# Optimization experiments

Hardware: AMD Instinct MI355X
Metric: run time of the kernel (lower is better)

## Reference

```python
import jax, jax.numpy as jnp
import numpy as np

N_NODES = 100000
N_EDGES = 1600000
IN_F = 128
HID_F = 128
OUT_F = 128
HEAD_HID = 128
HEAD_OUT = 64


def setup_inputs() -> dict:
    key = jax.random.key(0)
    ks = jax.random.split(key, 16)
    glorot = lambda k, i, o: jax.random.normal(k, (i, o), jnp.float32) * (2.0 / (i + o)) ** 0.5
    return {
        "x": jax.random.normal(ks[0], (N_NODES, IN_F), jnp.float32),
        "src": jax.random.randint(ks[1], (N_EDGES,), 0, N_NODES),
        "dst": jax.random.randint(ks[2], (N_EDGES,), 0, N_NODES),
        "eps1": jnp.zeros((), jnp.float32),
        "eps2": jnp.zeros((), jnp.float32),
        # mlp_fun1: in_feats -> hid -> hid
        "w11": glorot(ks[3], IN_F, HID_F), "b11": jnp.zeros((HID_F,), jnp.float32),
        "w12": glorot(ks[4], HID_F, HID_F), "b12": jnp.zeros((HID_F,), jnp.float32),
        # mlp_fun2: hid -> hid -> out_feats
        "w21": glorot(ks[5], HID_F, HID_F), "b21": jnp.zeros((HID_F,), jnp.float32),
        "w22": glorot(ks[6], HID_F, OUT_F), "b22": jnp.zeros((OUT_F,), jnp.float32),
        # head mlp: out_feats -> hidden_dim -> output_dim (sigmoid)
        "wm1": glorot(ks[7], OUT_F, HEAD_HID), "bm1": jnp.zeros((HEAD_HID,), jnp.float32),
        "wm2": glorot(ks[8], HEAD_HID, HEAD_OUT), "bm2": jnp.zeros((HEAD_OUT,), jnp.float32),
    }


def _mlp2(h, w1, b1, w2, b2):
    # 2-layer MLP: Linear -> ReLU -> Linear
    return jax.nn.relu(h @ w1 + b1) @ w2 + b2


def _gin_conv(x, src, dst, eps, w1, b1, w2, b2):
    # sum-aggregate over incoming edges, then MLP update (DGL GINConv, learn_eps)
    agg = jax.ops.segment_sum(x[src], dst, num_segments=x.shape[0])  # [N, d]
    return _mlp2((1.0 + eps) * x + agg, w1, b1, w2, b2)


def reference(x, src, dst, eps1, eps2, w11, b11, w12, b12,
              w21, b21, w22, b22, wm1, bm1, wm2, bm2):
    # dropout is identity in eval mode
    h = jax.nn.relu(_gin_conv(x, src, dst, eps1, w11, b11, w12, b12))
    h = jax.nn.relu(_gin_conv(h, src, dst, eps2, w21, b21, w22, b22))
    # head MLP producing per-node probabilities (consumed by log-prob loss)
    return jax.nn.sigmoid(_mlp2(h, wm1, bm1, wm2, bm2))  # [N, output_dim]
```

## Files before the change

kernel.cpp:

```cpp
#include <hip/hip_runtime.h>

static constexpr int NN = 100000;
static constexpr int NE = 1600000;
static constexpr int NBUK = (NN + 1023) / 1024;
static constexpr int BCAP = 20480;
static constexpr int SC_BLOCKS = 400;
static constexpr int SC_CH = NE / SC_BLOCKS;

typedef float     f32x4  __attribute__((ext_vector_type(4)));
typedef _Float16  f16x8  __attribute__((ext_vector_type(8)));

static constexpr float LO_SCALE  = 16384.0f;
static constexpr float LO_USCALE = 1.0f / 16384.0f;

__device__ __forceinline__ unsigned pkh(float x, float y){
  unsigned short a = __builtin_bit_cast(unsigned short, (_Float16)x);
  unsigned short b = __builtin_bit_cast(unsigned short, (_Float16)y);
  return (unsigned)a | ((unsigned)b << 16);
}
__device__ __forceinline__ float2 uph(unsigned u){
  _Float16 a = __builtin_bit_cast(_Float16, (unsigned short)(u & 0xffffu));
  _Float16 b = __builtin_bit_cast(_Float16, (unsigned short)(u >> 16));
  return make_float2((float)a, (float)b);
}

__global__ void k_pack(const float* __restrict__ w11, const float* __restrict__ w12,
                       const float* __restrict__ w21, const float* __restrict__ w22,
                       const float* __restrict__ wm1, const float* __restrict__ wm2,
                       unsigned short* __restrict__ p11, unsigned short* __restrict__ p12,
                       unsigned short* __restrict__ p21, unsigned short* __restrict__ p22,
                       unsigned short* __restrict__ pm1, unsigned short* __restrict__ pm2){
  int b = blockIdx.x, lane = threadIdx.x;
  const float* W; unsigned short* P; int NCT, f;
  if (b < 160){
    int m = b >> 5; f = b & 31; NCT = 8;
    W = (m==0)?w11:(m==1)?w12:(m==2)?w21:(m==3)?w22:wm1;
    P = (m==0)?p11:(m==1)?p12:(m==2)?p21:(m==3)?p22:pm1;
  } else { f = b - 160; NCT = 4; W = wm2; P = pm2; }
  int NC = NCT * 16;
  int kt = f / NCT, ct = f % NCT;
  int hidx = ct >> 2, ct4 = ct & 3;
  int k0 = kt*32 + ((lane>>4)*8), col = ct*16 + (lane&15);
  unsigned short* dh = P + (hidx<<14) + ((kt*4+ct4)<<10) + (lane<<3);
  unsigned short* dl = dh + 512;
  #pragma unroll
  for (int j=0;j<8;j++){
    float v = W[(size_t)(k0+j)*NC + col];
    _Float16 h = (_Float16)v;
    _Float16 l = (_Float16)((v - (float)h) * LO_SCALE);
    dh[j] = __builtin_bit_cast(unsigned short, h);
    dl[j] = __builtin_bit_cast(unsigned short, l);
  }
}

__global__ void k_cvt(const float* __restrict__ x, unsigned* __restrict__ xh, int n4){
  int i = blockIdx.x*256 + threadIdx.x;
  if (i < n4){
    float4 v = reinterpret_cast<const float4*>(x)[i];
    uint2 o; o.x = pkh(v.x, v.y); o.y = pkh(v.z, v.w);
    reinterpret_cast<uint2*>(xh)[i] = o;
  }
}

__global__ __launch_bounds__(256) void k_scatter1(const int* __restrict__ src,
                                                  const int* __restrict__ dst,
                                                  int* __restrict__ gbcur,
                                                  unsigned* __restrict__ tmp){
  __shared__ int hc[NBUK];
  __shared__ int hb[NBUK];
  int blk = blockIdx.x, t = threadIdx.x;
  int e0 = blk * SC_CH, e1 = e0 + SC_CH;
  for (int i=t;i<NBUK;i+=256) hc[i]=0;
  __syncthreads();
  for (int e=e0+t; e<e1; e+=256) atomicAdd(&hc[((unsigned)dst[e])>>10], 1);
  __syncthreads();
  for (int i=t;i<NBUK;i+=256){ int c = hc[i]; hb[i] = c ? atomicAdd(&gbcur[i], c) : 0; }
  __syncthreads();
  for (int i=t;i<NBUK;i+=256) hc[i]=0;
  __syncthreads();
  for (int e=e0+t; e<e1; e+=256){
    unsigned d = (unsigned)dst[e]; unsigned b = d>>10;
    int pos = hb[b] + atomicAdd(&hc[b], 1);
    if (pos < BCAP)
      tmp[(size_t)b*BCAP + pos] = ((unsigned)src[e] << 10) | (d & 1023u);
  }
}

__global__ __launch_bounds__(256) void k_fill2(const unsigned* __restrict__ tmp,
                                               const int* __restrict__ gbcur,
                                               int* __restrict__ eidx,
                                               int* __restrict__ rs, int* __restrict__ deg, int N){
  __shared__ int lh[1024];
  __shared__ int ls[1024];
  __shared__ int lc[1024];
  __shared__ int wsum[256];
  int b = blockIdx.x, t = threadIdx.x;
  int base = b*BCAP;
  int cnt = gbcur[b]; if (cnt > BCAP) cnt = BCAP;
  int nb0 = b*1024;
  for (int i=t;i<1024;i+=256){ lh[i]=0; lc[i]=0; }
  __syncthreads();
  for (int i=t; i<cnt; i+=256) atomicAdd(&lh[tmp[(size_t)base+i] & 1023u], 1);
  __syncthreads();
  int v4[4]; int sum = 0;
  #pragma unroll
  for (int j=0;j<4;j++){ v4[j] = lh[t*4+j]; sum += v4[j]; }
  wsum[t] = sum; __syncthreads();
  for (int off=1; off<256; off<<=1){
    int u = 0; if (t>=off) u = wsum[t-off];
    __syncthreads(); wsum[t] += u; __syncthreads();
  }
  int run = wsum[t] - sum;
  #pragma unroll
  for (int j=0;j<4;j++){ ls[t*4+j] = run; run += v4[j]; }
  __syncthreads();
  #pragma unroll
  for (int j=0;j<4;j++){
    int node = nb0 + t*4 + j;
    if (node < N){ deg[node] = v4[j]; rs[node] = base + ls[t*4+j]; }
  }
  __syncthreads();
  for (int i=t; i<cnt; i+=256){
    unsigned e = tmp[(size_t)base+i];
    int local = e & 1023u;
    int pos = atomicAdd(&lc[local], 1);
    eidx[base + ls[local] + pos] = (int)(e >> 10);
  }
}

__global__ __launch_bounds__(256) void k_agg(const unsigned* __restrict__ inp,
                                             unsigned* __restrict__ out,
                                             const float* __restrict__ epsp,
                                             const int* __restrict__ rs, const int* __restrict__ deg,
                                             const int* __restrict__ eidx, int N){
  int gw = (blockIdx.x*256 + threadIdx.x) >> 6;
  int lane = threadIdx.x & 63;
  if (gw >= N) return;
  float sc = 1.0f + *epsp;
  float2 v = uph(inp[(size_t)gw*64 + lane]);
  float a0 = sc * v.x, a1 = sc * v.y;
  int beg = rs[gw], d = deg[gw];
  int i = 0;
  for (; i+8 <= d; i += 8){
    unsigned u[8];
    #pragma unroll
    for (int j=0;j<8;j++) u[j] = inp[(size_t)eidx[beg+i+j]*64 + lane];
    #pragma unroll
    for (int j=0;j<8;j++){ float2 f = uph(u[j]); a0 += f.x; a1 += f.y; }
  }
  for (; i < d; ++i){
    float2 u = uph(inp[(size_t)eidx[beg+i]*64 + lane]);
    a0 += u.x; a1 += u.y;
  }
  out[(size_t)gw*64 + lane] = pkh(a0, a1);
}

static constexpr int HSTR = 136;
static constexpr int WSLICE = 32*HSTR;
static constexpr int WSL64 = 64*HSTR;

__device__ __forceinline__ void load_a_glob4(const _Float16* __restrict__ t, int rbase,
                                             int lane, int N, f16x8 a[4][4]){
  #pragma unroll
  for (int ms=0; ms<4; ++ms){
    int row = rbase + ms*16 + (lane & 15); if (row >= N) row = N - 1;
    const _Float16* ap = t + (size_t)row*128 + ((lane>>4)*8);
    #pragma unroll
    for (int kt=0;kt<4;kt++) a[ms][kt] = *reinterpret_cast<const f16x8*>(ap + kt*32);
  }
}
__device__ __forceinline__ void load_a_lds4(const _Float16* slice, int lane, f16x8 a[4][4]){
  int ko = (lane>>4)*8;
  #pragma unroll
  for (int ms=0; ms<4; ++ms){
    const _Float16* rp = slice + (ms*16 + (lane&15))*HSTR + ko;
    #pragma unroll
    for (int kt=0;kt<4;kt++) a[ms][kt] = *reinterpret_cast<const f16x8*>(rp + kt*32);
  }
}
__device__ __forceinline__ void half_relu64(const f16x8 a[4][4],
                                            const unsigned short* __restrict__ w,
                                            const float* __restrict__ bias,
                                            _Float16* slice, int lane, int hidx){
  const unsigned short* wb = w + (hidx<<14);
  int r0 = (lane>>4)*4, col0 = lane & 15;
  #pragma unroll
  for (int ct4=0; ct4<4; ++ct4){
    f32x4 c[4], d[4];
    #pragma unroll
    for (int m=0;m<4;m++){ c[m] = {0.f,0.f,0.f,0.f}; d[m] = {0.f,0.f,0.f,0.f}; }
    #pragma unroll
    for (int kt=0; kt<4; ++kt){
      const f16x8 bh = *reinterpret_cast<const f16x8*>(wb + ((kt*4+ct4)<<10) + (lane<<3));
      const f16x8 bl = *reinterpret_cast<const f16x8*>(wb + ((kt*4+ct4)<<10) + 512 + (lane<<3));
      #pragma unroll
      for (int m=0;m<4;m++){
        c[m] = __builtin_amdgcn_mfma_f32_16x16x32_f16(a[m][kt], bh, c[m], 0,0,0);
        d[m] = __builtin_amdgcn_mfma_f32_16x16x32_f16(a[m][kt], bl, d[m], 0,0,0);
      }
    }
    float bv = bias[hidx*64 + ct4*16 + col0];
    int cb = hidx*64 + ct4*16 + col0;
    #pragma unroll
    for (int m=0;m<4;m++){
      #pragma unroll
      for (int r=0;r<4;r++){
        float v = fmaxf(c[m][r] + d[m][r]*LO_USCALE + bv, 0.f);
        slice[(m*16 + r0 + r)*HSTR + cb] = (_Float16)v;
      }
    }
  }
}

__device__ __forceinline__ void load_a_glob2(const _Float16* __restrict__ t, int rbase,
                                             int lane, int N, f16x8 a[2][4]){
  #pragma unroll
  for (int ms=0; ms<2; ++ms){
    int row = rbase + ms*16 + (lane & 15); if (row >= N) row = N - 1;
    const _Float16* ap = t + (size_t)row*128 + ((lane>>4)*8);
    #pragma unroll
    for (int kt=0;kt<4;kt++) a[ms][kt] = *reinterpret_cast<const f16x8*>(ap + kt*32);
  }
}
__device__ __forceinline__ void load_a_lds2(const _Float16* slice, int lane, f16x8 a[2][4]){
  int ko = (lane>>4)*8;
  #pragma unroll
  for (int ms=0; ms<2; ++ms){
    const _Float16* rp = slice + (ms*16 + (lane&15))*HSTR + ko;
    #pragma unroll
    for (int kt=0;kt<4;kt++) a[ms][kt] = *reinterpret_cast<const f16x8*>(rp + kt*32);
  }
}
__device__ __forceinline__ void half_relu(const f16x8 a[2][4],
                                          const unsigned short* __restrict__ w,
                                          const float* __restrict__ bias,
                                          _Float16* slice, int lane, int hidx){
  const unsigned short* wb = w + (hidx<<14);
  int r0 = (lane>>4)*4, col0 = lane & 15;
  #pragma unroll
  for (int ct4=0; ct4<4; ++ct4){
    f32x4 c0={0.f,0.f,0.f,0.f}, c1={0.f,0.f,0.f,0.f};
    f32x4 d0={0.f,0.f,0.f,0.f}, d1={0.f,0.f,0.f,0.f};
    #pragma unroll
    for (int kt=0; kt<4; ++kt){
      const f16x8 bh = *reinterpret_cast<const f16x8*>(wb + ((kt*4+ct4)<<10) + (lane<<3));
      const f16x8 bl = *reinterpret_cast<const f16x8*>(wb + ((kt*4+ct4)<<10) + 512 + (lane<<3));
      c0 = __builtin_amdgcn_mfma_f32_16x16x32_f16(a[0][kt], bh, c0, 0,0,0);
      c1 = __builtin_amdgcn_mfma_f32_16x16x32_f16(a[1][kt], bh, c1, 0,0,0);
      d0 = __builtin_amdgcn_mfma_f32_16x16x32_f16(a[0][kt], bl, d0, 0,0,0);
      d1 = __builtin_amdgcn_mfma_f32_16x16x32_f16(a[1][kt], bl, d1, 0,0,0);
    }
    float bv = bias[hidx*64 + ct4*16 + col0];
    int cb = hidx*64 + ct4*16 + col0;
    #pragma unroll
    for (int r=0;r<4;r++){
      float v0 = fmaxf(c0[r] + d0[r]*LO_USCALE + bv, 0.f);
      float v1 = fmaxf(c1[r] + d1[r]*LO_USCALE + bv, 0.f);
      slice[(r0+r)*HSTR + cb]      = (_Float16)v0;
      slice[(16+r0+r)*HSTR + cb]   = (_Float16)v1;
    }
  }
}
__device__ __forceinline__ void head_sig(const f16x8 a[2][4],
                                         const unsigned short* __restrict__ w,
                                         const float* __restrict__ bias,
                                         float* fs, int lane){
  int r0 = (lane>>4)*4, col0 = lane & 15;
  #pragma unroll
  for (int ct4=0; ct4<4; ++ct4){
    f32x4 c0={0.f,0.f,0.f,0.f}, c1={0.f,0.f,0.f,0.f};
    f32x4 d0={0.f,0.f,0.f,0.f}, d1={0.f,0.f,0.f,0.f};
    #pragma unroll
    for (int kt=0; kt<4; ++kt){
      const f16x8 bh = *reinterpret_cast<const f16x8*>(w + ((kt*4+ct4)<<10) + (lane<<3));
      const f16x8 bl = *reinterpret_cast<const f16x8*>(w + ((kt*4+ct4)<<10) + 512 + (lane<<3));
      c0 = __builtin_amdgcn_mfma_f32_16x16x32_f16(a[0][kt], bh, c0, 0,0,0);
      c1 = __builtin_amdgcn_mfma_f32_16x16x32_f16(a[1][kt], bh, c1, 0,0,0);
      d0 = __builtin_amdgcn_mfma_f32_16x16x32_f16(a[0][kt], bl, d0, 0,0,0);
      d1 = __builtin_amdgcn_mfma_f32_16x16x32_f16(a[1][kt], bl, d1, 0,0,0);
    }
    float bv = bias[ct4*16 + col0];
    int cb = ct4*16 + col0;
    #pragma unroll
    for (int r=0;r<4;r++){
      float z0 = c0[r] + d0[r]*LO_USCALE + bv;
      float z1 = c1[r] + d1[r]*LO_USCALE + bv;
      fs[(r0+r)*68 + cb]    = 1.0f / (1.0f + __expf(-z0));
      fs[(16+r0+r)*68 + cb] = 1.0f / (1.0f + __expf(-z1));
    }
  }
}

__global__ __launch_bounds__(128) void k_mlp1(const _Float16* __restrict__ t,
    const unsigned short* __restrict__ w1, const float* __restrict__ b1,
    const unsigned short* __restrict__ w2, const float* __restrict__ b2,
    unsigned* __restrict__ h, int N){
  __shared__ _Float16 lds[2*WSL64];
  int tid = threadIdx.x, lane = tid & 63, wv = tid >> 6;
  _Float16* slice = lds + wv*WSL64;
  int rbase = blockIdx.x*128 + wv*64;
  f16x8 a[4][4];
  load_a_glob4(t, rbase, lane, N, a);
  half_relu64(a, w1, b1, slice, lane, 0);
  half_relu64(a, w1, b1, slice, lane, 1);
  load_a_lds4(slice, lane, a);
  half_relu64(a, w2, b2, slice, lane, 0);
  half_relu64(a, w2, b2, slice, lane, 1);
  for (int i=lane; i < 64*32; i += 64){
    int r = i >> 5, c = i & 31;
    if (rbase + r < N)
      reinterpret_cast<uint2*>(h)[(size_t)(rbase + r)*32 + c] =
        *reinterpret_cast<const uint2*>(slice + r*HSTR + c*4);
  }
}

__global__ __launch_bounds__(256) void k_mlp2_head(const _Float16* __restrict__ t,
    const unsigned short* __restrict__ w1, const float* __restrict__ b1,
    const unsigned short* __restrict__ w2, const float* __restrict__ b2,
    const unsigned short* __restrict__ w3, const float* __restrict__ b3,
    const unsigned short* __restrict__ w4, const float* __restrict__ b4,
    float* __restrict__ out, int N){
  __shared__ _Float16 lds[4*WSLICE];
  int tid = threadIdx.x, lane = tid & 63, wv = tid >> 6;
  _Float16* slice = lds + wv*WSLICE;
  int rbase = blockIdx.x*128 + wv*32;
  f16x8 a[2][4];
  load_a_glob2(t, rbase, lane, N, a);
  half_relu(a, w1, b1, slice, lane, 0);
  half_relu(a, w1, b1, slice, lane, 1);
  load_a_lds2(slice, lane, a);
  half_relu(a, w2, b2, slice, lane, 0);
  half_relu(a, w2, b2, slice, lane, 1);
  load_a_lds2(slice, lane, a);
  half_relu(a, w3, b3, slice, lane, 0);
  half_relu(a, w3, b3, slice, lane, 1);
  load_a_lds2(slice, lane, a);
  float* fs = reinterpret_cast<float*>(slice);
  head_sig(a, w4, b4, fs, lane);
  for (int i=lane; i < 32*16; i += 64){
    int r = i >> 4, c = i & 15;
    if (rbase + r < N){
      f32x4 o = *reinterpret_cast<const f32x4*>(fs + r*68 + c*4);
      __builtin_nontemporal_store(o,
        reinterpret_cast<f32x4*>(out) + (size_t)(rbase + r)*16 + c);
    }
  }
}

extern "C" void kernel_launch(void* const* d_in, const int* in_sizes, int n_in,
                              void* d_out, int out_size, void* d_ws, size_t ws_size,
                              hipStream_t stream) {
  const float* x   = (const float*)d_in[0];
  const int*   src = (const int*)  d_in[1];
  const int*   dst = (const int*)  d_in[2];
  const float* eps1= (const float*)d_in[3];
  const float* eps2= (const float*)d_in[4];
  const float* w11 = (const float*)d_in[5];  const float* b11 = (const float*)d_in[6];
  const float* w12 = (const float*)d_in[7];  const float* b12 = (const float*)d_in[8];
  const float* w21 = (const float*)d_in[9];  const float* b21 = (const float*)d_in[10];
  const float* w22 = (const float*)d_in[11]; const float* b22 = (const float*)d_in[12];
  const float* wm1 = (const float*)d_in[13]; const float* bm1 = (const float*)d_in[14];
  const float* wm2 = (const float*)d_in[15]; const float* bm2 = (const float*)d_in[16];

  char* ws = (char*)d_ws;
  size_t off = 0;
  auto alloc = [&](size_t bytes) -> void* {
    void* p = ws + off;
    off = (off + bytes + 255) & ~(size_t)255;
    return p;
  };
  unsigned* xh  = (unsigned*)alloc((size_t)NN*64*4);
  unsigned* B0  = (unsigned*)alloc((size_t)NN*64*4);
  unsigned* h1h = (unsigned*)alloc((size_t)NN*64*4);
  unsigned* tmp = (unsigned*)alloc((size_t)NBUK*BCAP*4);
  int* eidx = (int*)alloc((size_t)NBUK*BCAP*4);
  int* deg  = (int*)alloc((size_t)NN*4);
  int* rs   = (int*)alloc((size_t)NN*4);
  int* gbcur= (int*)alloc((size_t)NBUK*4);
  unsigned short* p11 = (unsigned short*)alloc(128*128*2*2);
  unsigned short* p12 = (unsigned short*)alloc(128*128*2*2);
  unsigned short* p21 = (unsigned short*)alloc(128*128*2*2);
  unsigned short* p22 = (unsigned short*)alloc(128*128*2*2);
  unsigned short* pm1 = (unsigned short*)alloc(128*128*2*2);
  unsigned short* pm2 = (unsigned short*)alloc(128*64*2*2);
  if (off > ws_size) return;

  hipMemsetAsync(gbcur, 0, (size_t)NBUK*4, stream);

  k_pack<<<176, 64, 0, stream>>>(w11,w12,w21,w22,wm1,wm2, p11,p12,p21,p22,pm1,pm2);
  k_cvt<<<(NN*32 + 255)/256, 256, 0, stream>>>(x, xh, NN*32);
  k_scatter1<<<SC_BLOCKS, 256, 0, stream>>>(src, dst, gbcur, tmp);
  k_fill2<<<NBUK, 256, 0, stream>>>(tmp, gbcur, eidx, rs, deg, NN);

  int mgrid = (NN + 127) / 128;
  k_agg<<<(NN+3)/4, 256, 0, stream>>>(xh, B0, eps1, rs, deg, eidx, NN);
  k_mlp1<<<mgrid, 128, 0, stream>>>((const _Float16*)B0, p11, b11, p12, b12, h1h, NN);
  k_agg<<<(NN+3)/4, 256, 0, stream>>>(h1h, B0, eps2, rs, deg, eidx, NN);
  k_mlp2_head<<<mgrid, 256, 0, stream>>>((const _Float16*)B0, p21, b21, p22, b22,
                                         pm1, bm1, pm2, bm2, (float*)d_out, NN);
}
```

Before: 293.1 us.

## Stage MLP weight chunks through double-buffered LDS in fused head kernel

Reorders the packed weight layout so each 16-column output chunk's four k-tiles are contiguous. In the fused MLP2+head kernel, those 8 KB chunks are now staged into double-buffered shared memory and shared by all four waves, instead of each wave reading them from global memory. The aim is to cut redundant global/L2 weight traffic per block. In exchange it adds a block-wide barrier per chunk (28 per block) and 16 KB of extra LDS, which may reduce occupancy.

Measured after the change: 291.8 us. About the same (-0.5%).

```diff
diff --git a/kernel.cpp b/kernel.cpp
--- a/kernel.cpp
+++ b/kernel.cpp
@@ -41,7 +41,7 @@
   int kt = f / NCT, ct = f % NCT;
   int hidx = ct >> 2, ct4 = ct & 3;
   int k0 = kt*32 + ((lane>>4)*8), col = ct*16 + (lane&15);
-  unsigned short* dh = P + (hidx<<14) + ((kt*4+ct4)<<10) + (lane<<3);
+  unsigned short* dh = P + (hidx<<14) + ((ct4*4+kt)<<10) + (lane<<3);
   unsigned short* dl = dh + 512;
   #pragma unroll
   for (int j=0;j<8;j++){
@@ -191,8 +191,8 @@
     for (int m=0;m<4;m++){ c[m] = {0.f,0.f,0.f,0.f}; d[m] = {0.f,0.f,0.f,0.f}; }
     #pragma unroll
     for (int kt=0; kt<4; ++kt){
-      const f16x8 bh = *reinterpret_cast<const f16x8*>(wb + ((kt*4+ct4)<<10) + (lane<<3));
-      const f16x8 bl = *reinterpret_cast<const f16x8*>(wb + ((kt*4+ct4)<<10) + 512 + (lane<<3));
+      const f16x8 bh = *reinterpret_cast<const f16x8*>(wb + ((ct4*4+kt)<<10) + (lane<<3));
+      const f16x8 bl = *reinterpret_cast<const f16x8*>(wb + ((ct4*4+kt)<<10) + 512 + (lane<<3));
       #pragma unroll
       for (int m=0;m<4;m++){
         c[m] = __builtin_amdgcn_mfma_f32_16x16x32_f16(a[m][kt], bh, c[m], 0,0,0);
@@ -231,63 +231,55 @@
     for (int kt=0;kt<4;kt++) a[ms][kt] = *reinterpret_cast<const f16x8*>(rp + kt*32);
   }
 }
-__device__ __forceinline__ void half_relu(const f16x8 a[2][4],
-                                          const unsigned short* __restrict__ w,
-                                          const float* __restrict__ bias,
-                                          _Float16* slice, int lane, int hidx){
-  const unsigned short* wb = w + (hidx<<14);
-  int r0 = (lane>>4)*4, col0 = lane & 15;
-  #pragma unroll
-  for (int ct4=0; ct4<4; ++ct4){
-    f32x4 c0={0.f,0.f,0.f,0.f}, c1={0.f,0.f,0.f,0.f};
-    f32x4 d0={0.f,0.f,0.f,0.f}, d1={0.f,0.f,0.f,0.f};
-    #pragma unroll
-    for (int kt=0; kt<4; ++kt){
-      const f16x8 bh = *reinterpret_cast<const f16x8*>(wb + ((kt*4+ct4)<<10) + (lane<<3));
-      const f16x8 bl = *reinterpret_cast<const f16x8*>(wb + ((kt*4+ct4)<<10) + 512 + (lane<<3));
-      c0 = __builtin_amdgcn_mfma_f32_16x16x32_f16(a[0][kt], bh, c0, 0,0,0);
-      c1 = __builtin_amdgcn_mfma_f32_16x16x32_f16(a[1][kt], bh, c1, 0,0,0);
-      d0 = __builtin_amdgcn_mfma_f32_16x16x32_f16(a[0][kt], bl, d0, 0,0,0);
-      d1 = __builtin_amdgcn_mfma_f32_16x16x32_f16(a[1][kt], bl, d1, 0,0,0);
-    }
-    float bv = bias[hidx*64 + ct4*16 + col0];
-    int cb = hidx*64 + ct4*16 + col0;
-    #pragma unroll
-    for (int r=0;r<4;r++){
-      float v0 = fmaxf(c0[r] + d0[r]*LO_USCALE + bv, 0.f);
-      float v1 = fmaxf(c1[r] + d1[r]*LO_USCALE + bv, 0.f);
-      slice[(r0+r)*HSTR + cb]      = (_Float16)v0;
-      slice[(16+r0+r)*HSTR + cb]   = (_Float16)v1;
-    }
-  }
-}
-__device__ __forceinline__ void head_sig(const f16x8 a[2][4],
-                                         const unsigned short* __restrict__ w,
-                                         const float* __restrict__ bias,
-                                         float* fs, int lane){
-  int r0 = (lane>>4)*4, col0 = lane & 15;
-  #pragma unroll
-  for (int ct4=0; ct4<4; ++ct4){
-    f32x4 c0={0.f,0.f,0.f,0.f}, c1={0.f,0.f,0.f,0.f};
-    f32x4 d0={0.f,0.f,0.f,0.f}, d1={0.f,0.f,0.f,0.f};
-    #pragma unroll
-    for (int kt=0; kt<4; ++kt){
-      const f16x8 bh = *reinterpret_cast<const f16x8*>(w + ((kt*4+ct4)<<10) + (lane<<3));
-      const f16x8 bl = *reinterpret_cast<const f16x8*>(w + ((kt*4+ct4)<<10) + 512 + (lane<<3));
-      c0 = __builtin_amdgcn_mfma_f32_16x16x32_f16(a[0][kt], bh, c0, 0,0,0);
-      c1 = __builtin_amdgcn_mfma_f32_16x16x32_f16(a[1][kt], bh, c1, 0,0,0);
-      d0 = __builtin_amdgcn_mfma_f32_16x16x32_f16(a[0][kt], bl, d0, 0,0,0);
-      d1 = __builtin_amdgcn_mfma_f32_16x16x32_f16(a[1][kt], bl, d1, 0,0,0);
-    }
-    float bv = bias[ct4*16 + col0];
-    int cb = ct4*16 + col0;
-    #pragma unroll
-    for (int r=0;r<4;r++){
-      float z0 = c0[r] + d0[r]*LO_USCALE + bv;
-      float z1 = c1[r] + d1[r]*LO_USCALE + bv;
-      fs[(r0+r)*68 + cb]    = 1.0f / (1.0f + __expf(-z0));
-      fs[(16+r0+r)*68 + cb] = 1.0f / (1.0f + __expf(-z1));
-    }
+
+__device__ __forceinline__ void stg(_Float16* d, const unsigned short* s, int tid){
+  reinterpret_cast<f16x8*>(d)[tid]       = reinterpret_cast<const f16x8*>(s)[tid];
+  reinterpret_cast<f16x8*>(d)[tid + 256] = reinterpret_cast<const f16x8*>(s)[tid + 256];
+}
+
+__device__ __forceinline__ void cchunk(const f16x8 a[2][4], const _Float16* wch,
+                                       float bv, _Float16* slice, int lane, int cb){
+  f32x4 c0={0.f,0.f,0.f,0.f}, c1={0.f,0.f,0.f,0.f};
+  f32x4 d0={0.f,0.f,0.f,0.f}, d1={0.f,0.f,0.f,0.f};
+  #pragma unroll
+  for (int kt=0; kt<4; ++kt){
+    const f16x8 bh = *reinterpret_cast<const f16x8*>(wch + (kt<<10) + (lane<<3));
+    const f16x8 bl = *reinterpret_cast<const f16x8*>(wch + (kt<<10) + 512 + (lane<<3));
+    c0 = __builtin_amdgcn_mfma_f32_16x16x32_f16(a[0][kt], bh, c0, 0,0,0);
+    c1 = __builtin_amdgcn_mfma_f32_16x16x32_f16(a[1][kt], bh, c1, 0,0,0);
+    d0 = __builtin_amdgcn_mfma_f32_16x16x32_f16(a[0][kt], bl, d0, 0,0,0);
+    d1 = __builtin_amdgcn_mfma_f32_16x16x32_f16(a[1][kt], bl, d1, 0,0,0);
+  }
+  int r0 = (lane>>4)*4;
+  #pragma unroll
+  for (int r=0;r<4;r++){
+    float v0 = fmaxf(c0[r] + d0[r]*LO_USCALE + bv, 0.f);
+    float v1 = fmaxf(c1[r] + d1[r]*LO_USCALE + bv, 0.f);
+    slice[(r0+r)*HSTR + cb]    = (_Float16)v0;
+    slice[(16+r0+r)*HSTR + cb] = (_Float16)v1;
+  }
+}
+
+__device__ __forceinline__ void cchunk_head(const f16x8 a[2][4], const _Float16* wch,
+                                            float bv, float* fs, int lane, int cb){
+  f32x4 c0={0.f,0.f,0.f,0.f}, c1={0.f,0.f,0.f,0.f};
+  f32x4 d0={0.f,0.f,0.f,0.f}, d1={0.f,0.f,0.f,0.f};
+  #pragma unroll
+  for (int kt=0; kt<4; ++kt){
+    const f16x8 bh = *reinterpret_cast<const f16x8*>(wch + (kt<<10) + (lane<<3));
+    const f16x8 bl = *reinterpret_cast<const f16x8*>(wch + (kt<<10) + 512 + (lane<<3));
+    c0 = __builtin_amdgcn_mfma_f32_16x16x32_f16(a[0][kt], bh, c0, 0,0,0);
+    c1 = __builtin_amdgcn_mfma_f32_16x16x32_f16(a[1][kt], bh, c1, 0,0,0);
+    d0 = __builtin_amdgcn_mfma_f32_16x16x32_f16(a[0][kt], bl, d0, 0,0,0);
+    d1 = __builtin_amdgcn_mfma_f32_16x16x32_f16(a[1][kt], bl, d1, 0,0,0);
+  }
+  int r0 = (lane>>4)*4;
+  #pragma unroll
+  for (int r=0;r<4;r++){
+    float z0 = c0[r] + d0[r]*LO_USCALE + bv;
+    float z1 = c1[r] + d1[r]*LO_USCALE + bv;
+    fs[(r0+r)*68 + cb]    = 1.0f / (1.0f + __expf(-z0));
+    fs[(16+r0+r)*68 + cb] = 1.0f / (1.0f + __expf(-z1));
   }
 }
 
@@ -321,22 +313,41 @@
     const unsigned short* __restrict__ w4, const float* __restrict__ b4,
     float* __restrict__ out, int N){
   __shared__ _Float16 lds[4*WSLICE];
+  __shared__ _Float16 wb0[4096];
+  __shared__ _Float16 wb1[4096];
   int tid = threadIdx.x, lane = tid & 63, wv = tid >> 6;
   _Float16* slice = lds + wv*WSLICE;
+  float* fs = reinterpret_cast<float*>(slice);
   int rbase = blockIdx.x*128 + wv*32;
+  int col0 = lane & 15;
   f16x8 a[2][4];
   load_a_glob2(t, rbase, lane, N, a);
-  half_relu(a, w1, b1, slice, lane, 0);
-  half_relu(a, w1, b1, slice, lane, 1);
-  load_a_lds2(slice, lane, a);
-  half_relu(a, w2, b2, slice, lane, 0);
-  half_relu(a, w2, b2, slice, lane, 1);
-  load_a_lds2(slice, lane, a);
-  half_relu(a, w3, b3, slice, lane, 0);
-  half_relu(a, w3, b3, slice, lane, 1);
-  load_a_lds2(slice, lane, a);
-  float* fs = reinterpret_cast<float*>(slice);
-  head_sig(a, w4, b4, fs, lane);
+  stg(wb0, w1, tid);
+  __syncthreads();
+  #pragma unroll
+  for (int i=0; i<28; ++i){
+    _Float16* cur = (i & 1) ? wb1 : wb0;
+    _Float16* nxt = (i & 1) ? wb0 : wb1;
+    if (i+1 < 28){
+      int j = i+1;
+      const unsigned short* s =
+        (j < 8)  ? (w1 + j*4096) :
+        (j < 16) ? (w2 + (j-8)*4096) :
+        (j < 24) ? (w3 + (j-16)*4096) :
+                   (w4 + (j-24)*4096);
+      stg(nxt, s, tid);
+    }
+    if (i < 24){
+      const float* bias = (i < 8) ? b1 : (i < 16) ? b2 : b3;
+      int cb = ((i & 7) << 4) + col0;
+      cchunk(a, cur, bias[cb], slice, lane, cb);
+    } else {
+      int cb = ((i & 3) << 4) + col0;
+      cchunk_head(a, cur, b4[cb], fs, lane, cb);
+    }
+    if (i == 7 || i == 15 || i == 23) load_a_lds2(slice, lane, a);
+    __syncthreads();
+  }
   for (int i=lane; i < 32*16; i += 64){
     int r = i >> 4, c = i & 15;
     if (rbase + r < N){
```
